# Optimization experiments

Measured on AMD Instinct MI355X. Metric: run time of the kernel, lower is better.

Reference implementation:

```python
import jax, jax.numpy as jnp
import numpy as np

B, S, D = 4, 1024, 1024
NH_M, INNER = 4, 2048          # mLSTM: 4 heads, proj_factor 2.0
DH_M = INNER // NH_M           # 512
QKV_BLK = 4                    # qkv_proj_blocksize
NH_S = 4
DH_S = D // NH_S               # 256
K = 4                          # causal conv1d kernel size
FF_UP = 1344                   # round_up(1.3*1024, 64)
OUT_EMO, OUT_SEN = 7, 3


def _ln(x, w, eps=1e-5):
    mu = x.mean(-1, keepdims=True)
    var = x.var(-1, keepdims=True)
    return (x - mu) * jax.lax.rsqrt(var + eps) * w


def _causal_conv1d(x, w, b):
    # x:(B,S,C), w:(C,K) depthwise causal conv
    C = x.shape[-1]
    xp = jnp.pad(x, ((0, 0), (K - 1, 0), (0, 0)))
    kern = w.T[:, None, :]  # (K,1,C)
    y = jax.lax.conv_general_dilated(xp, kern, (1,), 'VALID',
        dimension_numbers=('NWC', 'WIO', 'NWC'), feature_group_count=C)
    return y + b


def _headwise(x, w):
    # block-diagonal linear; x:(B,S,nb*bi), w:(nb,bo,bi)
    nb, bo, bi = w.shape
    xr = x.reshape(x.shape[0], x.shape[1], nb, bi)
    return jnp.einsum('bsni,noi->bsno', xr, w).reshape(x.shape[0], x.shape[1], nb * bo)


def _mh_layernorm(h, w, eps=1e-5):
    # h:(B,S,NH,DH): per-head layernorm, affine weight over NH*DH
    mu = h.mean(-1, keepdims=True)
    var = h.var(-1, keepdims=True)
    hn = (h - mu) * jax.lax.rsqrt(var + eps)
    return hn.reshape(h.shape[0], h.shape[1], -1) * w


def _mlstm_parallel(q, k, v, ig, fg, eps=1e-6):
    # q,k,v:(B,NH,S,DH); ig,fg:(B,NH,S). Stabilized parallel mLSTM (matrix memory).
    Sx, DH = q.shape[2], q.shape[3]
    lfc = jnp.cumsum(jax.nn.log_sigmoid(fg), axis=-1)            # (B,NH,S)
    logfg_mat = lfc[..., :, None] - lfc[..., None, :]            # (B,NH,S,S)
    mask = jnp.tril(jnp.ones((Sx, Sx), bool))
    logD = jnp.where(mask, logfg_mat + ig[..., None, :], -jnp.inf)
    maxD = logD.max(-1, keepdims=True)                           # finite (diagonal)
    Dm = jnp.exp(logD - maxD)
    qk = jnp.einsum('bhid,bhjd->bhij', q, k * (DH ** -0.5))
    C = qk * Dm
    norm = jnp.maximum(jnp.abs(C.sum(-1, keepdims=True)), jnp.exp(-maxD))
    return jnp.einsum('bhij,bhjd->bhid', C / (norm + eps), v)


def _slstm_scan(i_pre, f_pre, z_pre, o_pre, R, b):
    # gate preacts:(B,S,NH,DH); R:(NH,DH,4*DH) recurrent; b:(NH,4,DH)
    Bx, Sx, NH, DH = i_pre.shape
    z0 = jnp.zeros((Bx, NH, DH), i_pre.dtype)
    def step(carry, xs):
        c, n, h, m = carry
        ix, fx, zx, ox = xs
        ry = jnp.einsum('bhd,hdk->bhk', h, R).reshape(Bx, NH, 4, DH)
        ir = ix + ry[:, :, 0] + b[None, :, 0]
        fr = fx + ry[:, :, 1] + b[None, :, 1]
        zr = zx + ry[:, :, 2] + b[None, :, 2]
        og = ox + ry[:, :, 3] + b[None, :, 3]
        logfplusm = m + jax.nn.log_sigmoid(fr)
        m_new = jnp.maximum(ir, logfplusm)
        i_g = jnp.exp(ir - m_new)
        f_g = jnp.exp(logfplusm - m_new)
        c_new = f_g * c + i_g * jnp.tanh(zr)
        n_new = f_g * n + i_g
        h_new = jax.nn.sigmoid(og) * (c_new / (n_new + 1e-6))
        return (c_new, n_new, h_new, m_new), h_new
    xs = tuple(jnp.moveaxis(t, 1, 0) for t in (i_pre, f_pre, z_pre, o_pre))
    _, hs = jax.lax.scan(step, (z0, z0, z0, z0), xs)
    return jnp.moveaxis(hs, 0, 1)  # (B,S,NH,DH)


def _forward(x, m_ln_w, m_Wup, m_conv_w, m_conv_b, m_Wq, m_Wk, m_Wv, m_Wig, m_big,
             m_Wfg, m_bfg, m_mhln_w, m_skip, m_Wdown, s_ln_w, s_conv_w, s_conv_b,
             s_Wi, s_Wf, s_Wz, s_Wo, s_R, s_b, s_mhln_w, s_ffn_ln_w, s_Wup, s_Wdown2,
             post_ln_w, h_We, h_be, h_Ws, h_bs):
    Bx, Sx, _ = x.shape
    # ---- block 0: mLSTM block (pre-norm residual) ----
    res = x
    xn = _ln(x, m_ln_w)
    xi, z = jnp.split(xn @ m_Wup, 2, axis=-1)            # (B,S,INNER) each
    xc = jax.nn.silu(_causal_conv1d(xi, m_conv_w, m_conv_b))
    q = _headwise(xc, m_Wq)
    k = _headwise(xc, m_Wk)
    v = _headwise(xi, m_Wv)
    qkv = jnp.concatenate([q, k, v], axis=-1)            # (B,S,3*INNER)
    ig = (qkv @ m_Wig + m_big).transpose(0, 2, 1)        # (B,NH,S)
    fg = (qkv @ m_Wfg + m_bfg).transpose(0, 2, 1)
    th = lambda t: t.reshape(Bx, Sx, NH_M, DH_M).transpose(0, 2, 1, 3)
    h = _mlstm_parallel(th(q), th(k), th(v), ig, fg)     # (B,NH,S,DH)
    hn = _mh_layernorm(h.transpose(0, 2, 1, 3), m_mhln_w)
    x = res + ((hn + m_skip * xc) * jax.nn.silu(z)) @ m_Wdown

    # ---- block 1: sLSTM block + gated FFN ----
    res = x
    xn = _ln(x, s_ln_w)
    xc = jax.nn.silu(_causal_conv1d(xn, s_conv_w, s_conv_b))
    hw = lambda t, w: jnp.einsum('bshi,hoi->bsho', t.reshape(Bx, Sx, NH_S, DH_S), w)
    hs = _slstm_scan(hw(xc, s_Wi), hw(xc, s_Wf), hw(xn, s_Wz), hw(xn, s_Wo), s_R, s_b)
    x = res + _mh_layernorm(hs, s_mhln_w)
    g, u = jnp.split(_ln(x, s_ffn_ln_w) @ s_Wup, 2, axis=-1)
    x = x + (jax.nn.gelu(g) * u) @ s_Wdown2

    # ---- post-blocks norm, SELU, mean pool, classification head ----
    x = _ln(x, post_ln_w)
    feat = jnp.mean(jax.nn.selu(x), axis=1)              # (B,D)
    return jnp.concatenate([feat @ h_We + h_be, feat @ h_Ws + h_bs], axis=-1)


def setup_inputs():
    ks = iter(jax.random.split(jax.random.key(0), 48))
    r = lambda *s: jax.random.normal(next(ks), s, jnp.float32) * 0.02
    return {
        'x': jax.random.normal(next(ks), (B, S, D), jnp.float32),
        'm_ln_w': jnp.ones((D,), jnp.float32),
        'm_Wup': r(D, 2 * INNER),
        'm_conv_w': r(INNER, K),
        'm_conv_b': jnp.zeros((INNER,), jnp.float32),
        'm_Wq': r(INNER // QKV_BLK, QKV_BLK, QKV_BLK),
        'm_Wk': r(INNER // QKV_BLK, QKV_BLK, QKV_BLK),
        'm_Wv': r(INNER // QKV_BLK, QKV_BLK, QKV_BLK),
        'm_Wig': r(3 * INNER, NH_M),
        'm_big': jnp.zeros((NH_M,), jnp.float32),
        'm_Wfg': r(3 * INNER, NH_M),
        'm_bfg': jnp.zeros((NH_M,), jnp.float32),
        'm_mhln_w': jnp.ones((INNER,), jnp.float32),
        'm_skip': jnp.ones((INNER,), jnp.float32),
        'm_Wdown': r(INNER, D),
        's_ln_w': jnp.ones((D,), jnp.float32),
        's_conv_w': r(D, K),
        's_conv_b': jnp.zeros((D,), jnp.float32),
        's_Wi': r(NH_S, DH_S, DH_S),
        's_Wf': r(NH_S, DH_S, DH_S),
        's_Wz': r(NH_S, DH_S, DH_S),
        's_Wo': r(NH_S, DH_S, DH_S),
        's_R': r(NH_S, DH_S, 4 * DH_S),
        's_b': jnp.zeros((NH_S, 4, DH_S), jnp.float32),
        's_mhln_w': jnp.ones((D,), jnp.float32),
        's_ffn_ln_w': jnp.ones((D,), jnp.float32),
        's_Wup': r(D, 2 * FF_UP),
        's_Wdown2': r(FF_UP, D),
        'post_ln_w': jnp.ones((D,), jnp.float32),
        'h_We': r(D, OUT_EMO),
        'h_be': jnp.zeros((OUT_EMO,), jnp.float32),
        'h_Ws': r(D, OUT_SEN),
        'h_bs': jnp.zeros((OUT_SEN,), jnp.float32),
    }


def reference(x, m_ln_w, m_Wup, m_conv_w, m_conv_b, m_Wq, m_Wk, m_Wv, m_Wig, m_big,
              m_Wfg, m_bfg, m_mhln_w, m_skip, m_Wdown, s_ln_w, s_conv_w, s_conv_b,
              s_Wi, s_Wf, s_Wz, s_Wo, s_R, s_b, s_mhln_w, s_ffn_ln_w, s_Wup, s_Wdown2,
              post_ln_w, h_We, h_be, h_Ws, h_bs):
    return _forward(x, m_ln_w, m_Wup, m_conv_w, m_conv_b, m_Wq, m_Wk, m_Wv, m_Wig,
                    m_big, m_Wfg, m_bfg, m_mhln_w, m_skip, m_Wdown, s_ln_w, s_conv_w,
                    s_conv_b, s_Wi, s_Wf, s_Wz, s_Wo, s_R, s_b, s_mhln_w, s_ffn_ln_w,
                    s_Wup, s_Wdown2, post_ln_w, h_We, h_be, h_Ws, h_bs)
```

## Files before the change

### kernel.cpp

```cpp
#include <hip/hip_runtime.h>
#include <hip/hip_bf16.h>


#define DEV_INLINE __device__ __forceinline__

constexpr long OFF_XN = 0;
constexpr long OFF_UP = 4l << 20;
constexpr long OFF_XC = 20l << 20;
constexpr long OFF_HS = 24l << 20;
constexpr long OFF_H  = 28l << 20;
constexpr long OFF_X1 = 36l << 20;
constexpr long OFF_SM = 40l << 20;

typedef _Float16 f16x2 __attribute__((ext_vector_type(2)));

DEV_INLINE float wave_reduce_sum(float v) {
#pragma unroll
  for (int o = 32; o > 0; o >>= 1) v += __shfl_xor(v, o);
  return v;
}

DEV_INLINE float silu_f(float x) { return x / (1.f + expf(-x)); }
DEV_INLINE float selu_f(float x) {
  return 1.0507009873554805f * (x > 0.f ? x : 1.6732632423543772f * (expf(x) - 1.f));
}

DEV_INLINE float dot2u(unsigned h2, unsigned r2, float c) {
#if __has_builtin(__builtin_amdgcn_fdot2)
  return __builtin_amdgcn_fdot2(__builtin_bit_cast(f16x2, h2),
                                __builtin_bit_cast(f16x2, r2), c, false);
#else
  const f16x2 a = __builtin_bit_cast(f16x2, h2);
  const f16x2 b = __builtin_bit_cast(f16x2, r2);
  return c + (float)a[0] * (float)b[0] + (float)a[1] * (float)b[1];
#endif
}

__global__ __launch_bounds__(256) void ln1024_kernel(
    const float* __restrict__ in, const float* __restrict__ w,
    float* __restrict__ out, int applySelu) {
  __shared__ float sred[8];
  const int n = blockIdx.x, t = threadIdx.x;
  const long base = (long)n * 1024 + t * 4;
  float4 v = *(const float4*)&in[base];
  float s = v.x + v.y + v.z + v.w;
  s = wave_reduce_sum(s);
  const int wid = t >> 6;
  if ((t & 63) == 0) sred[wid] = s;
  __syncthreads();
  const float mu = (sred[0] + sred[1] + sred[2] + sred[3]) * (1.f / 1024.f);
  float4 d;
  d.x = v.x - mu; d.y = v.y - mu; d.z = v.z - mu; d.w = v.w - mu;
  float sq = d.x * d.x + d.y * d.y + d.z * d.z + d.w * d.w;
  sq = wave_reduce_sum(sq);
  if ((t & 63) == 0) sred[4 + wid] = sq;
  __syncthreads();
  const float var = (sred[4] + sred[5] + sred[6] + sred[7]) * (1.f / 1024.f);
  const float rstd = rsqrtf(var + 1e-5f);
  const float4 w4 = *(const float4*)&w[t * 4];
  float4 o4;
  o4.x = d.x * rstd * w4.x; o4.y = d.y * rstd * w4.y;
  o4.z = d.z * rstd * w4.z; o4.w = d.w * rstd * w4.w;
  if (applySelu) {
    o4.x = selu_f(o4.x); o4.y = selu_f(o4.y); o4.z = selu_f(o4.z); o4.w = selu_f(o4.w);
  }
  *(float4*)&out[base] = o4;
}

template <bool WT>
__global__ __launch_bounds__(256) void gemm_kernel(
    const float* __restrict__ A, int lda, long aZ,
    const float* __restrict__ W, int ldw, long wZ,
    const float* __restrict__ Res, int ldr, long rZ,
    float* __restrict__ C, int ldc, long cZ,
    int M, int N, int Kd) {
  __shared__ float As[8][128];
  __shared__ float Bs[8][132];
  const int bn = blockIdx.x * 128;
  const int bm = blockIdx.y * 128;
  A += (long)blockIdx.z * aZ;
  W += (long)blockIdx.z * wZ;
  C += (long)blockIdx.z * cZ;
  const float* Rp = Res ? Res + (long)blockIdx.z * rZ : nullptr;
  const int t = threadIdx.x;
  const int tx = t & 15, ty = t >> 4;

  float acc[8][8] = {};

  const int ar = t >> 1, ak = (t & 1) * 4;
  for (int k0 = 0; k0 < Kd; k0 += 8) {
    const float4 av = *(const float4*)&A[(long)(bm + ar) * lda + k0 + ak];
    float4 bv;
    int bk, bn4, bnr, bk4;
    if (!WT) {
      bk = t >> 5; bn4 = (t & 31) << 2;
      bv = *(const float4*)&W[(long)(k0 + bk) * ldw + bn + bn4];
    } else {
      bnr = t >> 1; bk4 = (t & 1) * 4;
      bv = *(const float4*)&W[(long)(bn + bnr) * ldw + k0 + bk4];
    }
    As[ak + 0][ar] = av.x; As[ak + 1][ar] = av.y;
    As[ak + 2][ar] = av.z; As[ak + 3][ar] = av.w;
    if (!WT) {
      *(float4*)&Bs[bk][bn4] = bv;
    } else {
      Bs[bk4 + 0][bnr] = bv.x; Bs[bk4 + 1][bnr] = bv.y;
      Bs[bk4 + 2][bnr] = bv.z; Bs[bk4 + 3][bnr] = bv.w;
    }
    __syncthreads();
#pragma unroll
    for (int kk = 0; kk < 8; ++kk) {
      float a0[8], b0[8];
      *(float4*)&a0[0] = *(const float4*)&As[kk][ty * 8];
      *(float4*)&a0[4] = *(const float4*)&As[kk][ty * 8 + 4];
      *(float4*)&b0[0] = *(const float4*)&Bs[kk][tx * 8];
      *(float4*)&b0[4] = *(const float4*)&Bs[kk][tx * 8 + 4];
#pragma unroll
      for (int i = 0; i < 8; ++i)
#pragma unroll
        for (int j = 0; j < 8; ++j) acc[i][j] += a0[i] * b0[j];
    }
    __syncthreads();
  }

  const int row0 = bm + ty * 8, col0 = bn + tx * 8;
#pragma unroll
  for (int i = 0; i < 8; ++i) {
#pragma unroll
    for (int jq = 0; jq < 8; jq += 4) {
      float4 o;
      o.x = acc[i][jq + 0]; o.y = acc[i][jq + 1];
      o.z = acc[i][jq + 2]; o.w = acc[i][jq + 3];
      if (Rp) {
        const float4 r4 = *(const float4*)&Rp[(long)(row0 + i) * ldr + col0 + jq];
        o.x += r4.x; o.y += r4.y; o.z += r4.z; o.w += r4.w;
      }
      *(float4*)&C[(long)(row0 + i) * ldc + col0 + jq] = o;
    }
  }
}

__global__ __launch_bounds__(256) void conv_silu_kernel(
    const float* __restrict__ in, int ld_in,
    const float* __restrict__ w, const float* __restrict__ bias,
    float* __restrict__ out, int ld_out, int C) {
  const int idx = blockIdx.x * 256 + threadIdx.x;
  const int gpr = C >> 2;
  const int n = idx / gpr;
  const int c = (idx - n * gpr) << 2;
  const int s = n & 1023;
  float4 acc = *(const float4*)&bias[c];
  const float* wc = &w[c * 4];
#pragma unroll
  for (int tap = 0; tap < 4; ++tap) {
    const int sp = s - 3 + tap;
    if (sp >= 0) {
      const float4 xv = *(const float4*)&in[(long)(n - 3 + tap) * ld_in + c];
      acc.x += xv.x * wc[0 + tap];
      acc.y += xv.y * wc[4 + tap];
      acc.z += xv.z * wc[8 + tap];
      acc.w += xv.w * wc[12 + tap];
    }
  }
  acc.x = silu_f(acc.x); acc.y = silu_f(acc.y);
  acc.z = silu_f(acc.z); acc.w = silu_f(acc.w);
  *(float4*)&out[(long)n * ld_out + c] = acc;
}

__global__ __launch_bounds__(256) void wtilde_kernel(
    const float* __restrict__ Wq, const float* __restrict__ Wk,
    const float* __restrict__ Wv, const float* __restrict__ Wig,
    const float* __restrict__ Wfg,
    float* __restrict__ wqk_ig, float* __restrict__ wv_ig,
    float* __restrict__ wqk_fg, float* __restrict__ wv_fg) {
  const int idx = blockIdx.x * 256 + threadIdx.x;
  const int c = idx >> 2, hm = idx & 3;
  const int bk = c >> 2, i = c & 3;
  float sqk_i = 0, sv_i = 0, sqk_f = 0, sv_f = 0;
#pragma unroll
  for (int o = 0; o < 4; ++o) {
    const float wq = Wq[(bk * 4 + o) * 4 + i];
    const float wk = Wk[(bk * 4 + o) * 4 + i];
    const float wv = Wv[(bk * 4 + o) * 4 + i];
    const int rq = bk * 4 + o;
    sqk_i += wq * Wig[rq * 4 + hm] + wk * Wig[(2048 + rq) * 4 + hm];
    sv_i  += wv * Wig[(4096 + rq) * 4 + hm];
    sqk_f += wq * Wfg[rq * 4 + hm] + wk * Wfg[(2048 + rq) * 4 + hm];
    sv_f  += wv * Wfg[(4096 + rq) * 4 + hm];
  }
  wqk_ig[idx] = sqk_i; wv_ig[idx] = sv_i;
  wqk_fg[idx] = sqk_f; wv_fg[idx] = sv_f;
}

__global__ __launch_bounds__(256) void igfg_kernel(
    const float* __restrict__ xc, const float* __restrict__ up,
    const float* __restrict__ wqk_ig, const float* __restrict__ wv_ig,
    const float* __restrict__ wqk_fg, const float* __restrict__ wv_fg,
    const float* __restrict__ big, const float* __restrict__ bfg,
    float* __restrict__ ig, float* __restrict__ fg) {
  __shared__ float red[4][8];
  const int n = blockIdx.x, t = threadIdx.x;
  float ai[4] = {0, 0, 0, 0}, af[4] = {0, 0, 0, 0};
  for (int c = t; c < 2048; c += 256) {
    const float xcv = xc[(long)n * 2048 + c];
    const float xiv = up[(long)n * 4096 + c];
    const float4 wiq = *(const float4*)&wqk_ig[c * 4];
    const float4 wiv = *(const float4*)&wv_ig[c * 4];
    const float4 wfq = *(const float4*)&wqk_fg[c * 4];
    const float4 wfv = *(const float4*)&wv_fg[c * 4];
    ai[0] += xcv * wiq.x + xiv * wiv.x;
    ai[1] += xcv * wiq.y + xiv * wiv.y;
    ai[2] += xcv * wiq.z + xiv * wiv.z;
    ai[3] += xcv * wiq.w + xiv * wiv.w;
    af[0] += xcv * wfq.x + xiv * wfv.x;
    af[1] += xcv * wfq.y + xiv * wfv.y;
    af[2] += xcv * wfq.z + xiv * wfv.z;
    af[3] += xcv * wfq.w + xiv * wfv.w;
  }
#pragma unroll
  for (int j = 0; j < 4; ++j) {
    ai[j] = wave_reduce_sum(ai[j]);
    af[j] = wave_reduce_sum(af[j]);
  }
  const int wid = t >> 6;
  if ((t & 63) == 0) {
#pragma unroll
    for (int j = 0; j < 4; ++j) { red[wid][j] = ai[j]; red[wid][4 + j] = af[j]; }
  }
  __syncthreads();
  if (t < 8) {
    const float v = red[0][t] + red[1][t] + red[2][t] + red[3][t];
    const int b = n >> 10, s = n & 1023;
    if (t < 4) ig[((long)b * 4 + t) * 1024 + s] = v + big[t];
    else       fg[((long)b * 4 + (t - 4)) * 1024 + s] = v + bfg[t - 4];
  }
}

__global__ __launch_bounds__(1024) void lfc_kernel(
    const float* __restrict__ fg, float* __restrict__ lfc) {
  __shared__ float sh[1024];
  const int bh = blockIdx.x, t = threadIdx.x;
  const float x = fg[(long)bh * 1024 + t];
  sh[t] = fminf(x, 0.f) - log1pf(expf(-fabsf(x)));
  __syncthreads();
  for (int off = 1; off < 1024; off <<= 1) {
    const float add = (t >= off) ? sh[t - off] : 0.f;
    __syncthreads();
    sh[t] += add;
    __syncthreads();
  }
  lfc[(long)bh * 1024 + t] = sh[t];
}

__global__ __launch_bounds__(256) void hv_inplace_kernel(
    float* __restrict__ up, const float* __restrict__ Wv) {
  const int idx = blockIdx.x * 256 + threadIdx.x;
  const int n = idx >> 9, bk = idx & 511;
  const long a = (long)n * 4096 + (bk << 2);
  const float4 xv = *(const float4*)&up[a];
  const float* wb = &Wv[bk << 4];
  float4 o;
  o.x = xv.x * wb[0]  + xv.y * wb[1]  + xv.z * wb[2]  + xv.w * wb[3];
  o.y = xv.x * wb[4]  + xv.y * wb[5]  + xv.z * wb[6]  + xv.w * wb[7];
  o.z = xv.x * wb[8]  + xv.y * wb[9]  + xv.z * wb[10] + xv.w * wb[11];
  o.w = xv.x * wb[12] + xv.y * wb[13] + xv.z * wb[14] + xv.w * wb[15];
  *(float4*)&up[a] = o;
}

__global__ __launch_bounds__(256) void mlstm_attn_kernel(
    const float* __restrict__ xc, const float* __restrict__ up,
    const float* __restrict__ Wq, const float* __restrict__ Wk,
    const float* __restrict__ lfc, const float* __restrict__ igv,
    float* __restrict__ hout) {
  __shared__ float q_s[32][516];
  __shared__ float kv_s[32][516];
  __shared__ float p_s[32][36];
  __shared__ float lfci_s[32], lfcj_s[32], igj_s[32];
  const int t = threadIdx.x;
  const int ti = t >> 5, tj = t & 31;
  const int i0 = blockIdx.x * 32;
  const int bh = blockIdx.y;
  const int b = bh >> 2, h = bh & 3;
  const float kscale = 0.04419417382415922f;

  for (int idx = t; idx < 32 * 128; idx += 256) {
    const int r = idx >> 7, g = idx & 127;
    const float4 xv =
        *(const float4*)&xc[((long)(b * 1024 + i0 + r)) * 2048 + h * 512 + (g << 2)];
    const float* wb = Wq + ((h * 128 + g) << 4);
    float4 q4;
    q4.x = xv.x * wb[0]  + xv.y * wb[1]  + xv.z * wb[2]  + xv.w * wb[3];
    q4.y = xv.x * wb[4]  + xv.y * wb[5]  + xv.z * wb[6]  + xv.w * wb[7];
    q4.z = xv.x * wb[8]  + xv.y * wb[9]  + xv.z * wb[10] + xv.w * wb[11];
    q4.w = xv.x * wb[12] + xv.y * wb[13] + xv.z * wb[14] + xv.w * wb[15];
    *(float4*)&q_s[r][g << 2] = q4;
  }
  if (t < 32) lfci_s[t] = lfc[(long)bh * 1024 + i0 + t];

  const int r0 = ti * 4;
  float m_run[4], ssum[4], accv[4][16];
#pragma unroll
  for (int e = 0; e < 4; ++e) {
    m_run[e] = -INFINITY; ssum[e] = 0.f;
#pragma unroll
    for (int u = 0; u < 16; ++u) accv[e][u] = 0.f;
  }

  for (int j0 = 0; j0 <= i0; j0 += 32) {
    __syncthreads();
    for (int idx = t; idx < 32 * 128; idx += 256) {
      const int r = idx >> 7, g = idx & 127;
      const float4 xv =
          *(const float4*)&xc[((long)(b * 1024 + j0 + r)) * 2048 + h * 512 + (g << 2)];
      const float* wb = Wk + ((h * 128 + g) << 4);
      float4 k4;
      k4.x = (xv.x * wb[0]  + xv.y * wb[1]  + xv.z * wb[2]  + xv.w * wb[3])  * kscale;
      k4.y = (xv.x * wb[4]  + xv.y * wb[5]  + xv.z * wb[6]  + xv.w * wb[7])  * kscale;
      k4.z = (xv.x * wb[8]  + xv.y * wb[9]  + xv.z * wb[10] + xv.w * wb[11]) * kscale;
      k4.w = (xv.x * wb[12] + xv.y * wb[13] + xv.z * wb[14] + xv.w * wb[15]) * kscale;
      *(float4*)&kv_s[r][g << 2] = k4;
    }
    if (t < 32) {
      lfcj_s[t] = lfc[(long)bh * 1024 + j0 + t];
      igj_s[t] = igv[(long)bh * 1024 + j0 + t];
    }
    __syncthreads();

    float sv[4] = {0.f, 0.f, 0.f, 0.f};
#pragma unroll 2
    for (int d = 0; d < 512; d += 4) {
      const float4 kv = *(const float4*)&kv_s[tj][d];
#pragma unroll
      for (int e = 0; e < 4; ++e) {
        const float4 qv = *(const float4*)&q_s[r0 + e][d];
        sv[e] += qv.x * kv.x + qv.y * kv.y + qv.z * kv.z + qv.w * kv.w;
      }
    }
    const float lfcj = lfcj_s[tj], igj = igj_s[tj];
    float mt[4], logd[4];
    bool valid[4];
#pragma unroll
    for (int e = 0; e < 4; ++e) {
      valid[e] = (j0 + tj) <= (i0 + r0 + e);
      logd[e] = lfci_s[r0 + e] - lfcj + igj;
      mt[e] = valid[e] ? logd[e] : -INFINITY;
    }
#pragma unroll
    for (int o = 16; o > 0; o >>= 1) {
#pragma unroll
      for (int e = 0; e < 4; ++e) mt[e] = fmaxf(mt[e], __shfl_xor(mt[e], o));
    }
    float p[4];
#pragma unroll
    for (int e = 0; e < 4; ++e) {
      const float mn = fmaxf(m_run[e], mt[e]);
      const float scale = __expf(m_run[e] - mn);
      m_run[e] = mn;
      p[e] = valid[e] ? sv[e] * __expf(logd[e] - mn) : 0.f;
      float ps = p[e];
#pragma unroll
      for (int o = 16; o > 0; o >>= 1) ps += __shfl_xor(ps, o);
      ssum[e] = ssum[e] * scale + ps;
#pragma unroll
      for (int u = 0; u < 16; ++u) accv[e][u] *= scale;
      p_s[r0 + e][tj] = p[e];
    }
    __syncthreads();

    for (int idx = t; idx < 32 * 128; idx += 256) {
      const int r = idx >> 7, g = idx & 127;
      const float4 vv =
          *(const float4*)&up[((long)(b * 1024 + j0 + r)) * 4096 + h * 512 + (g << 2)];
      *(float4*)&kv_s[r][g << 2] = vv;
    }
    __syncthreads();

#pragma unroll 2
    for (int j = 0; j < 32; ++j) {
      const float pj0 = p_s[r0 + 0][j];
      const float pj1 = p_s[r0 + 1][j];
      const float pj2 = p_s[r0 + 2][j];
      const float pj3 = p_s[r0 + 3][j];
#pragma unroll
      for (int u = 0; u < 16; ++u) {
        const float vv = kv_s[j][tj + (u << 5)];
        accv[0][u] += pj0 * vv;
        accv[1][u] += pj1 * vv;
        accv[2][u] += pj2 * vv;
        accv[3][u] += pj3 * vv;
      }
    }
  }

#pragma unroll
  for (int e = 0; e < 4; ++e) {
    const float norm = fmaxf(fabsf(ssum[e]), __expf(-m_run[e]));
    const float inv = 1.f / (norm + 1e-6f);
    const long rowbase = ((long)(b * 1024 + i0 + r0 + e)) * 2048 + h * 512;
#pragma unroll
    for (int u = 0; u < 16; ++u) hout[rowbase + tj + (u << 5)] = accv[e][u] * inv;
  }
}

__global__ __launch_bounds__(128) void mhgate_kernel(
    float* __restrict__ hbuf, const float* __restrict__ mhw,
    const float* __restrict__ skip, const float* __restrict__ xc,
    const float* __restrict__ up) {
  __shared__ float sred[4];
  const int nh = blockIdx.x, t = threadIdx.x;
  const int n = nh >> 2, hd = nh & 3;
  const long base = (long)n * 2048 + hd * 512 + t * 4;
  const float4 v = *(const float4*)&hbuf[base];
  float s = wave_reduce_sum(v.x + v.y + v.z + v.w);
  if ((t & 63) == 0) sred[t >> 6] = s;
  __syncthreads();
  const float mu = (sred[0] + sred[1]) * (1.f / 512.f);
  float4 d;
  d.x = v.x - mu; d.y = v.y - mu; d.z = v.z - mu; d.w = v.w - mu;
  float sq = wave_reduce_sum(d.x * d.x + d.y * d.y + d.z * d.z + d.w * d.w);
  if ((t & 63) == 0) sred[2 + (t >> 6)] = sq;
  __syncthreads();
  const float rstd = rsqrtf((sred[2] + sred[3]) * (1.f / 512.f) + 1e-5f);
  const int ch = hd * 512 + t * 4;
  const float4 w4 = *(const float4*)&mhw[ch];
  const float4 sk4 = *(const float4*)&skip[ch];
  const float4 xc4 = *(const float4*)&xc[(long)n * 2048 + ch];
  const float4 z4 = *(const float4*)&up[(long)n * 4096 + 2048 + ch];
  float4 o;
  o.x = (d.x * rstd * w4.x + sk4.x * xc4.x) * silu_f(z4.x);
  o.y = (d.y * rstd * w4.y + sk4.y * xc4.y) * silu_f(z4.y);
  o.z = (d.z * rstd * w4.z + sk4.z * xc4.z) * silu_f(z4.z);
  o.w = (d.w * rstd * w4.w + sk4.w * xc4.w) * silu_f(z4.w);
  *(float4*)&hbuf[base] = o;
}

__global__ __launch_bounds__(256) void rpack_kernel(
    const float* __restrict__ R, uint4* __restrict__ Rp) {
  const int idx = blockIdx.x * 256 + threadIdx.x;
  const int hd = idx >> 15, rem = idx & 32767;
  const int d8 = rem >> 10, col = rem & 1023;
  const float* p = R + ((long)(hd * 256 + d8 * 8)) * 1024 + col;
  unsigned short hw[8];
#pragma unroll
  for (int k = 0; k < 8; ++k)
    hw[k] = __builtin_bit_cast(unsigned short, (_Float16)p[(long)k * 1024]);
  uint4 o;
  o.x = (unsigned)hw[0] | ((unsigned)hw[1] << 16);
  o.y = (unsigned)hw[2] | ((unsigned)hw[3] << 16);
  o.z = (unsigned)hw[4] | ((unsigned)hw[5] << 16);
  o.w = (unsigned)hw[6] | ((unsigned)hw[7] << 16);
  Rp[idx] = o;
}

__global__ __launch_bounds__(1024) void slstm_scan_kernel(
    const float* __restrict__ gi, const float* __restrict__ gf,
    const float* __restrict__ gz, const float* __restrict__ go,
    const uint4* __restrict__ Rp, const float* __restrict__ bias,
    float* __restrict__ hsout) {
  __shared__ uint4 h16q[32];
  __shared__ float ry[1024];
  const int t = threadIdx.x;
  const int b = blockIdx.x >> 2, hd = blockIdx.x & 3;
  const uint4* Rc = Rp + (long)hd * 32768 + t;
  float c = 0.f, nn = 0.f, m = 0.f;
  float bi = 0, bf = 0, bz = 0, bo = 0;
  float gii = 0, gfv = 0, gzv = 0, gov = 0;
  if (t < 256) {
    ((_Float16*)h16q)[t] = (_Float16)0.f;
    bi = bias[(hd * 4 + 0) * 256 + t];
    bf = bias[(hd * 4 + 1) * 256 + t];
    bz = bias[(hd * 4 + 2) * 256 + t];
    bo = bias[(hd * 4 + 3) * 256 + t];
    const long pb0 = ((long)(b * 1024)) * 1024 + hd * 256 + t;
    gii = gi[pb0]; gfv = gf[pb0]; gzv = gz[pb0]; gov = go[pb0];
  }
  __syncthreads();
  for (int s = 0; s < 1024; ++s) {
    float acc = 0.f;
#pragma unroll 8
    for (int d8 = 0; d8 < 32; ++d8) {
      const uint4 rv = Rc[d8 * 1024];
      const uint4 hv = h16q[d8];
      acc = dot2u(hv.x, rv.x, acc);
      acc = dot2u(hv.y, rv.y, acc);
      acc = dot2u(hv.z, rv.z, acc);
      acc = dot2u(hv.w, rv.w, acc);
    }
    ry[t] = acc;
    float ni = 0, nf = 0, nz = 0, no = 0;
    if (t < 256 && s < 1023) {
      const long pb1 = ((long)(b * 1024 + s + 1)) * 1024 + hd * 256 + t;
      ni = gi[pb1]; nf = gf[pb1]; nz = gz[pb1]; no = go[pb1];
    }
    __syncthreads();
    if (t < 256) {
      const long pb = ((long)(b * 1024 + s)) * 1024 + hd * 256 + t;
      const float ir = gii + ry[t] + bi;
      const float fr = gfv + ry[256 + t] + bf;
      const float zr = gzv + ry[512 + t] + bz;
      const float og = gov + ry[768 + t] + bo;
      const float lsf = fminf(fr, 0.f) - log1pf(expf(-fabsf(fr)));
      const float lfm = m + lsf;
      const float mn = fmaxf(ir, lfm);
      const float igate = expf(ir - mn);
      const float fgate = expf(lfm - mn);
      c = fgate * c + igate * tanhf(zr);
      nn = fgate * nn + igate;
      const float hv = (1.f / (1.f + expf(-og))) * (c / (nn + 1e-6f));
      m = mn;
      ((_Float16*)h16q)[t] = (_Float16)hv;
      hsout[pb] = hv;
    }
    gii = ni; gfv = nf; gzv = nz; gov = no;
    __syncthreads();
  }
}

__global__ __launch_bounds__(64) void mhres_kernel(
    const float* __restrict__ hs, const float* __restrict__ w,
    const float* __restrict__ x1, float* __restrict__ x2) {
  const int nh = blockIdx.x, t = threadIdx.x;
  const int n = nh >> 2, hd = nh & 3;
  const long base = (long)n * 1024 + hd * 256 + t * 4;
  const float4 v = *(const float4*)&hs[base];
  const float mu = wave_reduce_sum(v.x + v.y + v.z + v.w) * (1.f / 256.f);
  float4 d;
  d.x = v.x - mu; d.y = v.y - mu; d.z = v.z - mu; d.w = v.w - mu;
  const float var =
      wave_reduce_sum(d.x * d.x + d.y * d.y + d.z * d.z + d.w * d.w) * (1.f / 256.f);
  const float rstd = rsqrtf(var + 1e-5f);
  const float4 w4 = *(const float4*)&w[hd * 256 + t * 4];
  const float4 r4 = *(const float4*)&x1[base];
  float4 o;
  o.x = r4.x + d.x * rstd * w4.x;
  o.y = r4.y + d.y * rstd * w4.y;
  o.z = r4.z + d.z * rstd * w4.z;
  o.w = r4.w + d.w * rstd * w4.w;
  *(float4*)&x2[base] = o;
}

__global__ __launch_bounds__(256) void geglu_kernel(float* __restrict__ ffn) {
  const int idx = blockIdx.x * 256 + threadIdx.x;
  const int n = idx / 1344, j = idx % 1344;
  const long base = (long)n * 2688;
  const float g = ffn[base + j];
  const float u = ffn[base + 1344 + j];
  const float t3 = 0.7978845608028654f * (g + 0.044715f * g * g * g);
  ffn[base + j] = 0.5f * g * (1.f + tanhf(t3)) * u;
}

__global__ __launch_bounds__(256) void colmean_kernel(
    const float* __restrict__ tmp, float* __restrict__ feat) {
  const int b = blockIdx.x >> 2;
  const int ch = ((blockIdx.x & 3) << 8) + threadIdx.x;
  const float* p = tmp + (long)b * 1024 * 1024 + ch;
  float s = 0.f;
#pragma unroll 4
  for (int si = 0; si < 1024; ++si) s += p[(long)si * 1024];
  feat[b * 1024 + ch] = s * (1.f / 1024.f);
}

__global__ __launch_bounds__(256) void head_kernel(
    const float* __restrict__ feat, const float* __restrict__ We,
    const float* __restrict__ be, const float* __restrict__ Ws,
    const float* __restrict__ bs, float* __restrict__ out) {
  __shared__ float sred[4];
  const int o = blockIdx.x, t = threadIdx.x;
  const int b = o / 10, j = o % 10;
  const float* wcol;
  int ld;
  float bias;
  if (j < 7) { wcol = We + j; ld = 7; bias = be[j]; }
  else       { wcol = Ws + (j - 7); ld = 3; bias = bs[j - 7]; }
  float s = 0.f;
  for (int d = t; d < 1024; d += 256) s += feat[b * 1024 + d] * wcol[d * ld];
  s = wave_reduce_sum(s);
  if ((t & 63) == 0) sred[t >> 6] = s;
  __syncthreads();
  if (t == 0) out[o] = sred[0] + sred[1] + sred[2] + sred[3] + bias;
}

extern "C" void kernel_launch(void* const* d_in, const int* in_sizes, int n_in,
                              void* d_out, int out_size, void* d_ws, size_t ws_size,
                              hipStream_t stream) {
  (void)in_sizes; (void)n_in; (void)out_size; (void)ws_size;
  const float* x        = (const float*)d_in[0];
  const float* m_ln_w   = (const float*)d_in[1];
  const float* m_Wup    = (const float*)d_in[2];
  const float* m_conv_w = (const float*)d_in[3];
  const float* m_conv_b = (const float*)d_in[4];
  const float* m_Wq     = (const float*)d_in[5];
  const float* m_Wk     = (const float*)d_in[6];
  const float* m_Wv     = (const float*)d_in[7];
  const float* m_Wig    = (const float*)d_in[8];
  const float* m_big    = (const float*)d_in[9];
  const float* m_Wfg    = (const float*)d_in[10];
  const float* m_bfg    = (const float*)d_in[11];
  const float* m_mhln_w = (const float*)d_in[12];
  const float* m_skip   = (const float*)d_in[13];
  const float* m_Wdown  = (const float*)d_in[14];
  const float* s_ln_w   = (const float*)d_in[15];
  const float* s_conv_w = (const float*)d_in[16];
  const float* s_conv_b = (const float*)d_in[17];
  const float* s_Wi     = (const float*)d_in[18];
  const float* s_Wf     = (const float*)d_in[19];
  const float* s_Wz     = (const float*)d_in[20];
  const float* s_Wo     = (const float*)d_in[21];
  const float* s_R      = (const float*)d_in[22];
  const float* s_b      = (const float*)d_in[23];
  const float* s_mhln_w = (const float*)d_in[24];
  const float* s_ffn_ln_w = (const float*)d_in[25];
  const float* s_Wup    = (const float*)d_in[26];
  const float* s_Wdown2 = (const float*)d_in[27];
  const float* post_ln_w = (const float*)d_in[28];
  const float* h_We     = (const float*)d_in[29];
  const float* h_be     = (const float*)d_in[30];
  const float* h_Ws     = (const float*)d_in[31];
  const float* h_bs     = (const float*)d_in[32];
  float* out = (float*)d_out;
  float* ws = (float*)d_ws;

  float* xn = ws + OFF_XN;
  float* up = ws + OFF_UP;
  float* xc = ws + OFF_XC;
  float* hsbuf = ws + OFF_HS;
  float* hb = ws + OFF_H;
  float* x1 = ws + OFF_X1;
  float* wqk_ig = ws + OFF_SM;
  float* wv_ig  = wqk_ig + 8192;
  float* wqk_fg = wqk_ig + 16384;
  float* wv_fg  = wqk_ig + 24576;
  float* igb    = ws + OFF_SM + 32768;
  float* fgb    = igb + 16384;
  float* lfcb   = igb + 32768;
  float* feat   = igb + 49152;

  ln1024_kernel<<<4096, 256, 0, stream>>>(x, m_ln_w, xn, 0);
  gemm_kernel<false><<<dim3(32, 32, 1), 256, 0, stream>>>(
      xn, 1024, 0, m_Wup, 4096, 0, nullptr, 0, 0, up, 4096, 0, 4096, 4096, 1024);
  conv_silu_kernel<<<(4096 * 512) / 256, 256, 0, stream>>>(
      up, 4096, m_conv_w, m_conv_b, xc, 2048, 2048);
  wtilde_kernel<<<32, 256, 0, stream>>>(m_Wq, m_Wk, m_Wv, m_Wig, m_Wfg,
                                        wqk_ig, wv_ig, wqk_fg, wv_fg);
  igfg_kernel<<<4096, 256, 0, stream>>>(xc, up, wqk_ig, wv_ig, wqk_fg, wv_fg,
                                        m_big, m_bfg, igb, fgb);
  lfc_kernel<<<16, 1024, 0, stream>>>(fgb, lfcb);
  hv_inplace_kernel<<<8192, 256, 0, stream>>>(up, m_Wv);
  mlstm_attn_kernel<<<dim3(32, 16), 256, 0, stream>>>(
      xc, up, m_Wq, m_Wk, lfcb, igb, hb);
  mhgate_kernel<<<16384, 128, 0, stream>>>(hb, m_mhln_w, m_skip, xc, up);
  gemm_kernel<false><<<dim3(8, 32, 1), 256, 0, stream>>>(
      hb, 2048, 0, m_Wdown, 1024, 0, x, 1024, 0, x1, 1024, 0, 4096, 1024, 2048);

  ln1024_kernel<<<4096, 256, 0, stream>>>(x1, s_ln_w, xn, 0);
  conv_silu_kernel<<<(4096 * 256) / 256, 256, 0, stream>>>(
      xn, 1024, s_conv_w, s_conv_b, xc, 1024, 1024);
  float* gi = up;
  float* gf = up + (4l << 20);
  float* gz = up + (8l << 20);
  float* go = up + (12l << 20);
  gemm_kernel<true><<<dim3(2, 32, 4), 256, 0, stream>>>(
      xc, 1024, 256, s_Wi, 256, 65536, nullptr, 0, 0, gi, 1024, 256, 4096, 256, 256);
  gemm_kernel<true><<<dim3(2, 32, 4), 256, 0, stream>>>(
      xc, 1024, 256, s_Wf, 256, 65536, nullptr, 0, 0, gf, 1024, 256, 4096, 256, 256);
  gemm_kernel<true><<<dim3(2, 32, 4), 256, 0, stream>>>(
      xn, 1024, 256, s_Wz, 256, 65536, nullptr, 0, 0, gz, 1024, 256, 4096, 256, 256);
  gemm_kernel<true><<<dim3(2, 32, 4), 256, 0, stream>>>(
      xn, 1024, 256, s_Wo, 256, 65536, nullptr, 0, 0, go, 1024, 256, 4096, 256, 256);
  uint4* Rpacked = (uint4*)xn;
  rpack_kernel<<<512, 256, 0, stream>>>(s_R, Rpacked);
  slstm_scan_kernel<<<16, 1024, 0, stream>>>(gi, gf, gz, go, Rpacked, s_b, hsbuf);
  mhres_kernel<<<16384, 64, 0, stream>>>(hsbuf, s_mhln_w, x1, hb);
  float* x2 = hb;

  ln1024_kernel<<<4096, 256, 0, stream>>>(x2, s_ffn_ln_w, xn, 0);
  float* ffn = up;
  gemm_kernel<false><<<dim3(21, 32, 1), 256, 0, stream>>>(
      xn, 1024, 0, s_Wup, 2688, 0, nullptr, 0, 0, ffn, 2688, 0, 4096, 2688, 1024);
  geglu_kernel<<<(4096 * 1344) / 256, 256, 0, stream>>>(ffn);
  gemm_kernel<false><<<dim3(8, 32, 1), 256, 0, stream>>>(
      ffn, 2688, 0, s_Wdown2, 1024, 0, x2, 1024, 0, x1, 1024, 0, 4096, 1024, 1344);
  float* x3 = x1;

  ln1024_kernel<<<4096, 256, 0, stream>>>(x3, post_ln_w, xn, 1);
  colmean_kernel<<<16, 256, 0, stream>>>(xn, feat);
  head_kernel<<<40, 256, 0, stream>>>(feat, h_We, h_be, h_Ws, h_bs, out);
}
```

Before: 8.002 ms.

## Replace fp32 SIMT GEMM with bf16 MFMA GEMM using swizzled shared tiles

Replaces the scalar fp32 outer-product GEMM with a kernel that converts A and W tiles to bf16 while staging them in LDS, using an XOR-swizzled layout. It then computes 128x128 tiles with 16x16x32 bf16 MFMA instructions, four waves each owning a 64x64 sub-tile. All dense projections (mLSTM up/down, sLSTM gate projections, FFN up/down) switch to it. The aim is to move the matmul FLOPs onto the matrix cores, at the cost of bf16 input rounding and a scalar per-element epilogue store.

```diff
diff --git a/kernel.cpp b/kernel.cpp
--- a/kernel.cpp
+++ b/kernel.cpp
@@ -13,6 +13,8 @@
 constexpr long OFF_SM = 40l << 20;
 
 typedef _Float16 f16x2 __attribute__((ext_vector_type(2)));
+typedef short bf16x8 __attribute__((ext_vector_type(8)));
+typedef float f32x4 __attribute__((ext_vector_type(4)));
 
 DEV_INLINE float wave_reduce_sum(float v) {
 #pragma unroll
@@ -23,6 +25,14 @@
 DEV_INLINE float silu_f(float x) { return x / (1.f + expf(-x)); }
 DEV_INLINE float selu_f(float x) {
   return 1.0507009873554805f * (x > 0.f ? x : 1.6732632423543772f * (expf(x) - 1.f));
+}
+
+DEV_INLINE unsigned short f2bf(float f) {
+  unsigned u = __float_as_uint(f);
+  return (unsigned short)((u + 0x7fffu + ((u >> 16) & 1u)) >> 16);
+}
+DEV_INLINE unsigned pk2(float a, float b) {
+  return (unsigned)f2bf(a) | ((unsigned)f2bf(b) << 16);
 }
 
 DEV_INLINE float dot2u(unsigned h2, unsigned r2, float c) {
@@ -67,75 +77,109 @@
   *(float4*)&out[base] = o4;
 }
 
+DEV_INLINE int idx16(int r, int kg) { return r * 4 + (kg ^ (r & 3)); }
+
 template <bool WT>
-__global__ __launch_bounds__(256) void gemm_kernel(
+__global__ __launch_bounds__(256) void gemm_mfma_kernel(
     const float* __restrict__ A, int lda, long aZ,
     const float* __restrict__ W, int ldw, long wZ,
     const float* __restrict__ Res, int ldr, long rZ,
-    float* __restrict__ C, int ldc, long cZ,
-    int M, int N, int Kd) {
-  __shared__ float As[8][128];
-  __shared__ float Bs[8][132];
-  const int bn = blockIdx.x * 128;
-  const int bm = blockIdx.y * 128;
+    float* __restrict__ C, int ldc, long cZ, int Kd) {
+  __shared__ __align__(16) short As[4096];
+  __shared__ __align__(16) short Bs[4096];
+  const int t = threadIdx.x;
+  const int lane = t & 63, wv = t >> 6;
+  const int wr = wv >> 1, wc = wv & 1;
+  const int lr = lane & 15, lk = lane >> 4;
+  const int bn = blockIdx.x * 128, bm = blockIdx.y * 128;
   A += (long)blockIdx.z * aZ;
   W += (long)blockIdx.z * wZ;
   C += (long)blockIdx.z * cZ;
   const float* Rp = Res ? Res + (long)blockIdx.z * rZ : nullptr;
-  const int t = threadIdx.x;
-  const int tx = t & 15, ty = t >> 4;
-
-  float acc[8][8] = {};
-
-  const int ar = t >> 1, ak = (t & 1) * 4;
-  for (int k0 = 0; k0 < Kd; k0 += 8) {
-    const float4 av = *(const float4*)&A[(long)(bm + ar) * lda + k0 + ak];
-    float4 bv;
-    int bk, bn4, bnr, bk4;
-    if (!WT) {
-      bk = t >> 5; bn4 = (t & 31) << 2;
-      bv = *(const float4*)&W[(long)(k0 + bk) * ldw + bn + bn4];
+
+  f32x4 acc[4][4];
+#pragma unroll
+  for (int i = 0; i < 4; ++i)
+#pragma unroll
+    for (int j = 0; j < 4; ++j) acc[i][j] = (f32x4){0.f, 0.f, 0.f, 0.f};
+
+  const int ar = t >> 1, ah = t & 1;
+  const int bk = t >> 3, bng = (t & 7) * 16;
+
+  for (int k0 = 0; k0 < Kd; k0 += 32) {
+    {
+      const float* ap = &A[(long)(bm + ar) * lda + k0 + ah * 16];
+      const float4 v0 = *(const float4*)&ap[0];
+      const float4 v1 = *(const float4*)&ap[4];
+      const float4 v2 = *(const float4*)&ap[8];
+      const float4 v3 = *(const float4*)&ap[12];
+      uint4 p0, p1;
+      p0.x = pk2(v0.x, v0.y); p0.y = pk2(v0.z, v0.w);
+      p0.z = pk2(v1.x, v1.y); p0.w = pk2(v1.z, v1.w);
+      p1.x = pk2(v2.x, v2.y); p1.y = pk2(v2.z, v2.w);
+      p1.z = pk2(v3.x, v3.y); p1.w = pk2(v3.z, v3.w);
+      *(uint4*)&As[idx16(ar, ah * 2 + 0) * 8] = p0;
+      *(uint4*)&As[idx16(ar, ah * 2 + 1) * 8] = p1;
+    }
+    if (WT) {
+      const float* wp = &W[(long)(bn + ar) * ldw + k0 + ah * 16];
+      const float4 v0 = *(const float4*)&wp[0];
+      const float4 v1 = *(const float4*)&wp[4];
+      const float4 v2 = *(const float4*)&wp[8];
+      const float4 v3 = *(const float4*)&wp[12];
+      uint4 p0, p1;
+      p0.x = pk2(v0.x, v0.y); p0.y = pk2(v0.z, v0.w);
+      p0.z = pk2(v1.x, v1.y); p0.w = pk2(v1.z, v1.w);
+      p1.x = pk2(v2.x, v2.y); p1.y = pk2(v2.z, v2.w);
+      p1.z = pk2(v3.x, v3.y); p1.w = pk2(v3.z, v3.w);
+      *(uint4*)&Bs[idx16(ar, ah * 2 + 0) * 8] = p0;
+      *(uint4*)&Bs[idx16(ar, ah * 2 + 1) * 8] = p1;
     } else {
-      bnr = t >> 1; bk4 = (t & 1) * 4;
-      bv = *(const float4*)&W[(long)(bn + bnr) * ldw + k0 + bk4];
-    }
-    As[ak + 0][ar] = av.x; As[ak + 1][ar] = av.y;
-    As[ak + 2][ar] = av.z; As[ak + 3][ar] = av.w;
-    if (!WT) {
-      *(float4*)&Bs[bk][bn4] = bv;
-    } else {
-      Bs[bk4 + 0][bnr] = bv.x; Bs[bk4 + 1][bnr] = bv.y;
-      Bs[bk4 + 2][bnr] = bv.z; Bs[bk4 + 3][bnr] = bv.w;
-    }
-    __syncthreads();
-#pragma unroll
-    for (int kk = 0; kk < 8; ++kk) {
-      float a0[8], b0[8];
-      *(float4*)&a0[0] = *(const float4*)&As[kk][ty * 8];
-      *(float4*)&a0[4] = *(const float4*)&As[kk][ty * 8 + 4];
-      *(float4*)&b0[0] = *(const float4*)&Bs[kk][tx * 8];
-      *(float4*)&b0[4] = *(const float4*)&Bs[kk][tx * 8 + 4];
-#pragma unroll
-      for (int i = 0; i < 8; ++i)
-#pragma unroll
-        for (int j = 0; j < 8; ++j) acc[i][j] += a0[i] * b0[j];
-    }
-    __syncthreads();
-  }
-
-  const int row0 = bm + ty * 8, col0 = bn + tx * 8;
-#pragma unroll
-  for (int i = 0; i < 8; ++i) {
-#pragma unroll
-    for (int jq = 0; jq < 8; jq += 4) {
-      float4 o;
-      o.x = acc[i][jq + 0]; o.y = acc[i][jq + 1];
-      o.z = acc[i][jq + 2]; o.w = acc[i][jq + 3];
-      if (Rp) {
-        const float4 r4 = *(const float4*)&Rp[(long)(row0 + i) * ldr + col0 + jq];
-        o.x += r4.x; o.y += r4.y; o.z += r4.z; o.w += r4.w;
+      const float* wp = &W[(long)(k0 + bk) * ldw + bn + bng];
+      const float4 v0 = *(const float4*)&wp[0];
+      const float4 v1 = *(const float4*)&wp[4];
+      const float4 v2 = *(const float4*)&wp[8];
+      const float4 v3 = *(const float4*)&wp[12];
+      const int kg = bk >> 3, ke = bk & 7;
+      float vv[16];
+      *(float4*)&vv[0] = v0; *(float4*)&vv[4] = v1;
+      *(float4*)&vv[8] = v2; *(float4*)&vv[12] = v3;
+#pragma unroll
+      for (int j = 0; j < 16; ++j)
+        Bs[idx16(bng + j, kg) * 8 + ke] = (short)f2bf(vv[j]);
+    }
+    __syncthreads();
+
+    bf16x8 afr[4], bfr[4];
+#pragma unroll
+    for (int mi = 0; mi < 4; ++mi)
+      afr[mi] = *(const bf16x8*)&As[idx16(wr * 64 + mi * 16 + lr, lk) * 8];
+#pragma unroll
+    for (int ni = 0; ni < 4; ++ni)
+      bfr[ni] = *(const bf16x8*)&Bs[idx16(wc * 64 + ni * 16 + lr, lk) * 8];
+#pragma unroll
+    for (int mi = 0; mi < 4; ++mi)
+#pragma unroll
+      for (int ni = 0; ni < 4; ++ni)
+        acc[mi][ni] = __builtin_amdgcn_mfma_f32_16x16x32_bf16(
+            afr[mi], bfr[ni], acc[mi][ni], 0, 0, 0);
+    __syncthreads();
+  }
+
+#pragma unroll
+  for (int mi = 0; mi < 4; ++mi) {
+    const int row0 = bm + wr * 64 + mi * 16 + lk * 4;
+#pragma unroll
+    for (int i = 0; i < 4; ++i) {
+      const long cb = (long)(row0 + i) * ldc;
+      const long rb = Rp ? (long)(row0 + i) * ldr : 0;
+#pragma unroll
+      for (int ni = 0; ni < 4; ++ni) {
+        const int col = bn + wc * 64 + ni * 16 + lr;
+        float v = acc[mi][ni][i];
+        if (Rp) v += Rp[rb + col];
+        C[cb + col] = v;
       }
-      *(float4*)&C[(long)(row0 + i) * ldc + col0 + jq] = o;
     }
   }
 }
@@ -636,8 +680,8 @@
   float* feat   = igb + 49152;
 
   ln1024_kernel<<<4096, 256, 0, stream>>>(x, m_ln_w, xn, 0);
-  gemm_kernel<false><<<dim3(32, 32, 1), 256, 0, stream>>>(
-      xn, 1024, 0, m_Wup, 4096, 0, nullptr, 0, 0, up, 4096, 0, 4096, 4096, 1024);
+  gemm_mfma_kernel<false><<<dim3(32, 32, 1), 256, 0, stream>>>(
+      xn, 1024, 0, m_Wup, 4096, 0, nullptr, 0, 0, up, 4096, 0, 1024);
   conv_silu_kernel<<<(4096 * 512) / 256, 256, 0, stream>>>(
       up, 4096, m_conv_w, m_conv_b, xc, 2048, 2048);
   wtilde_kernel<<<32, 256, 0, stream>>>(m_Wq, m_Wk, m_Wv, m_Wig, m_Wfg,
@@ -649,8 +693,8 @@
   mlstm_attn_kernel<<<dim3(32, 16), 256, 0, stream>>>(
       xc, up, m_Wq, m_Wk, lfcb, igb, hb);
   mhgate_kernel<<<16384, 128, 0, stream>>>(hb, m_mhln_w, m_skip, xc, up);
-  gemm_kernel<false><<<dim3(8, 32, 1), 256, 0, stream>>>(
-      hb, 2048, 0, m_Wdown, 1024, 0, x, 1024, 0, x1, 1024, 0, 4096, 1024, 2048);
+  gemm_mfma_kernel<false><<<dim3(8, 32, 1), 256, 0, stream>>>(
+      hb, 2048, 0, m_Wdown, 1024, 0, x, 1024, 0, x1, 1024, 0, 2048);
 
   ln1024_kernel<<<4096, 256, 0, stream>>>(x1, s_ln_w, xn, 0);
   conv_silu_kernel<<<(4096 * 256) / 256, 256, 0, stream>>>(
@@ -659,14 +703,14 @@
   float* gf = up + (4l << 20);
   float* gz = up + (8l << 20);
   float* go = up + (12l << 20);
-  gemm_kernel<true><<<dim3(2, 32, 4), 256, 0, stream>>>(
-      xc, 1024, 256, s_Wi, 256, 65536, nullptr, 0, 0, gi, 1024, 256, 4096, 256, 256);
-  gemm_kernel<true><<<dim3(2, 32, 4), 256, 0, stream>>>(
-      xc, 1024, 256, s_Wf, 256, 65536, nullptr, 0, 0, gf, 1024, 256, 4096, 256, 256);
-  gemm_kernel<true><<<dim3(2, 32, 4), 256, 0, stream>>>(
-      xn, 1024, 256, s_Wz, 256, 65536, nullptr, 0, 0, gz, 1024, 256, 4096, 256, 256);
-  gemm_kernel<true><<<dim3(2, 32, 4), 256, 0, stream>>>(
-      xn, 1024, 256, s_Wo, 256, 65536, nullptr, 0, 0, go, 1024, 256, 4096, 256, 256);
+  gemm_mfma_kernel<true><<<dim3(2, 32, 4), 256, 0, stream>>>(
+      xc, 1024, 256, s_Wi, 256, 65536, nullptr, 0, 0, gi, 1024, 256, 256);
+  gemm_mfma_kernel<true><<<dim3(2, 32, 4), 256, 0, stream>>>(
+      xc, 1024, 256, s_Wf, 256, 65536, nullptr, 0, 0, gf, 1024, 256, 256);
+  gemm_mfma_kernel<true><<<dim3(2, 32, 4), 256, 0, stream>>>(
+      xn, 1024, 256, s_Wz, 256, 65536, nullptr, 0, 0, gz, 1024, 256, 256);
+  gemm_mfma_kernel<true><<<dim3(2, 32, 4), 256, 0, stream>>>(
+      xn, 1024, 256, s_Wo, 256, 65536, nullptr, 0, 0, go, 1024, 256, 256);
   uint4* Rpacked = (uint4*)xn;
   rpack_kernel<<<512, 256, 0, stream>>>(s_R, Rpacked);
   slstm_scan_kernel<<<16, 1024, 0, stream>>>(gi, gf, gz, go, Rpacked, s_b, hsbuf);
@@ -675,11 +719,11 @@
 
   ln1024_kernel<<<4096, 256, 0, stream>>>(x2, s_ffn_ln_w, xn, 0);
   float* ffn = up;
-  gemm_kernel<false><<<dim3(21, 32, 1), 256, 0, stream>>>(
-      xn, 1024, 0, s_Wup, 2688, 0, nullptr, 0, 0, ffn, 2688, 0, 4096, 2688, 1024);
+  gemm_mfma_kernel<false><<<dim3(21, 32, 1), 256, 0, stream>>>(
+      xn, 1024, 0, s_Wup, 2688, 0, nullptr, 0, 0, ffn, 2688, 0, 1024);
   geglu_kernel<<<(4096 * 1344) / 256, 256, 0, stream>>>(ffn);
-  gemm_kernel<false><<<dim3(8, 32, 1), 256, 0, stream>>>(
-      ffn, 2688, 0, s_Wdown2, 1024, 0, x2, 1024, 0, x1, 1024, 0, 4096, 1024, 1344);
+  gemm_mfma_kernel<false><<<dim3(8, 32, 1), 256, 0, stream>>>(
+      ffn, 2688, 0, s_Wdown2, 1024, 0, x2, 1024, 0, x1, 1024, 0, 1344);
   float* x3 = x1;
 
   ln1024_kernel<<<4096, 256, 0, stream>>>(x3, post_ln_w, xn, 1);
```

New measurement: 6.995 ms. 1.14x faster.
